# Optimization experiments

Hardware: AMD Instinct MI355X
Metric: run time of the kernel (lower is better)

## Reference

```python
import jax, jax.numpy as jnp
import numpy as np
import math

B, S = 2, 2048
V, D, H, L, DFF = 1024, 512, 8, 6, 2048
DK = D // H
EPS = 1e-5


def _pos_encoding(seq_len, d_model, dtype):
    pos = jnp.arange(seq_len, dtype=jnp.float32)[:, None]
    div = jnp.exp(jnp.arange(0, d_model, 2, dtype=jnp.float32) * (-math.log(10000.0) / d_model))
    pe = jnp.zeros((seq_len, d_model), dtype=jnp.float32)
    pe = pe.at[:, 0::2].set(jnp.sin(pos * div))
    pe = pe.at[:, 1::2].set(jnp.cos(pos * div))
    return pe.astype(dtype)


def _layernorm(x, w, b):
    mu = jnp.mean(x, axis=-1, keepdims=True)
    var = jnp.mean(jnp.square(x - mu), axis=-1, keepdims=True)
    return (x - mu) * jax.lax.rsqrt(var + EPS) * w + b


def setup_inputs() -> dict:
    key = jax.random.key(0)
    ks = jax.random.split(key, 20)
    s = 0.02
    inp = {
        "input_ids": jax.random.randint(ks[0], (B, S), 1, V),
        "emb": jax.random.normal(ks[1], (V, D)) * s,
        # linear weights stored (in, out) so y = x @ W + b
        "wq": jax.random.normal(ks[2], (L, D, D)) * s,
        "bq": jnp.zeros((L, D)),
        "wk": jax.random.normal(ks[3], (L, D, D)) * s,
        "bk": jnp.zeros((L, D)),
        "wv": jax.random.normal(ks[4], (L, D, D)) * s,
        "bv": jnp.zeros((L, D)),
        "wo": jax.random.normal(ks[5], (L, D, D)) * (s / math.sqrt(2 * L)),
        "bo": jnp.zeros((L, D)),
        "ln1_w": jnp.ones((L, D)), "ln1_b": jnp.zeros((L, D)),
        "ln2_w": jnp.ones((L, D)), "ln2_b": jnp.zeros((L, D)),
        "w1": jax.random.normal(ks[6], (L, D, DFF)) * s,
        "b1": jnp.zeros((L, DFF)),
        "w2": jax.random.normal(ks[7], (L, DFF, D)) * (s / math.sqrt(2 * L)),
        "b2": jnp.zeros((L, D)),
        "out_w": jax.random.normal(ks[8], (D, V)) * s,
        "out_b": jnp.zeros((V,)),
    }
    return inp


def reference(input_ids, emb, wq, bq, wk, bk, wv, bv, wo, bo,
              ln1_w, ln1_b, ln2_w, ln2_b, w1, b1, w2, b2, out_w, out_b):
    pad_mask = (input_ids != 0)                              # [B,S] attend where True
    x = emb[input_ids]                                       # [B,S,D]
    x = x + _pos_encoding(S, D, x.dtype)[None, :, :]
    causal = jnp.tril(jnp.ones((S, S), dtype=bool))          # [S,S]
    mask = causal[None, None, :, :] & pad_mask[:, None, None, :]  # [B,1,S,S]
    scale = 1.0 / math.sqrt(DK)
    for l in range(L):
        h = _layernorm(x, ln1_w[l], ln1_b[l])
        q = (h @ wq[l] + bq[l]).reshape(B, S, H, DK)
        k = (h @ wk[l] + bk[l]).reshape(B, S, H, DK)
        v = (h @ wv[l] + bv[l]).reshape(B, S, H, DK)
        scores = jnp.einsum('bqhd,bkhd->bhqk', q, k) * scale
        scores = jnp.where(mask, scores, -jnp.inf)
        attn = jax.nn.softmax(scores, axis=-1)
        o = jnp.einsum('bhqk,bkhd->bqhd', attn, v).reshape(B, S, D)
        x = o @ wo[l] + bo[l]                                # NOTE: no residual on attention (faithful)
        h2 = _layernorm(x, ln2_w[l], ln2_b[l])
        ff = jax.nn.relu(h2 @ w1[l] + b1[l]) @ w2[l] + b2[l]
        x = x + ff
    logits = x @ out_w + out_b                               # [B,S,V]
    return logits
```

## Files before the change

kernel.cpp:

```cpp
#include <hip/hip_runtime.h>
#include <hip/hip_bf16.h>

#define B_ 2
#define S_ 2048
#define V_ 1024
#define D_ 512
#define H_ 8
#define L_ 6
#define DFF_ 2048
#define DK_ 64
#define MROWS (B_*S_)
#define NEGINF (-__builtin_inff())

typedef __hip_bfloat16 bf16;
typedef __bf16 bf16x8 __attribute__((ext_vector_type(8)));
typedef float f32x4 __attribute__((ext_vector_type(4)));
typedef unsigned short us8 __attribute__((ext_vector_type(8)));
typedef unsigned short us2 __attribute__((ext_vector_type(2)));

__device__ __forceinline__ float bf2f(unsigned short u) {
    return __uint_as_float(((unsigned int)u) << 16);
}
__device__ __forceinline__ unsigned short f2b(float x) {
    unsigned int u = __float_as_uint(x);
    return (unsigned short)((u + 0x7FFFu + ((u >> 16) & 1u)) >> 16);
}
__device__ __forceinline__ float ldin(const void* p, size_t i, int bf) {
    return bf ? bf2f(((const unsigned short*)p)[i]) : ((const float*)p)[i];
}

__global__ void detect_kernel(const unsigned int* __restrict__ w, int* __restrict__ flag) {
    if (threadIdx.x == 0) flag[0] = (w[0] == 0x3F800000u) ? 0 : 1;
}

__global__ __launch_bounds__(256) void embed_kernel(const int* __restrict__ ids,
        const void* __restrict__ emb, float* __restrict__ x, const int* __restrict__ dtf)
{
    const int bf = dtf[0];
    int tid = blockIdx.x * 256 + threadIdx.x;
    int d = tid % D_;
    int bs = tid / D_;
    int s = bs % S_;
    int id = ids[bs];
    float e = ldin(emb, (size_t)id * D_ + d, bf);
    int i2 = d & ~1;
    float div = expf((float)i2 * (-9.210340371976184f / (float)D_));
    float ang = (float)s * div;
    float pe = (d & 1) ? cosf(ang) : sinf(ang);
    x[tid] = e + pe;
}

__global__ __launch_bounds__(256) void ln_kernel(const float* __restrict__ x,
        const void* __restrict__ w, const void* __restrict__ b, size_t off,
        unsigned short* __restrict__ out, const int* __restrict__ dtf)
{
    const int bf = dtf[0];
    __shared__ float red[256];
    const int row = blockIdx.x;
    const int tid = threadIdx.x;
    const float* xr = x + (size_t)row * D_;
    float v0 = xr[tid], v1 = xr[tid + 256];
    red[tid] = v0 + v1; __syncthreads();
    for (int s = 128; s > 0; s >>= 1) { if (tid < s) red[tid] += red[tid + s]; __syncthreads(); }
    float mu = red[0] * (1.f / D_); __syncthreads();
    float d0 = v0 - mu, d1 = v1 - mu;
    red[tid] = d0 * d0 + d1 * d1; __syncthreads();
    for (int s = 128; s > 0; s >>= 1) { if (tid < s) red[tid] += red[tid + s]; __syncthreads(); }
    float var = red[0] * (1.f / D_);
    float rstd = rsqrtf(var + 1e-5f);
    unsigned short* orow = out + (size_t)row * D_;
    orow[tid]       = f2b(d0 * rstd * ldin(w, off + tid, bf)       + ldin(b, off + tid, bf));
    orow[tid + 256] = f2b(d1 * rstd * ldin(w, off + tid + 256, bf) + ldin(b, off + tid + 256, bf));
}

__device__ __forceinline__ void tr_tile(const void* src, size_t off, int K, int N,
        unsigned short* dst, int k0, int n0, int bf, unsigned short (*T)[72])
{
    const int t = threadIdx.x;
    const int r = t >> 2, c = (t & 3) * 16;
    size_t e = off + (size_t)(k0 + r) * N + n0 + c;
    us8 u0, u1;
    if (bf) {
        u0 = *(const us8*)((const unsigned short*)src + e);
        u1 = *(const us8*)((const unsigned short*)src + e + 8);
    } else {
        const float* p = (const float*)src + e;
        float4 f0 = *(const float4*)p, f1 = *(const float4*)(p + 4);
        float4 f2 = *(const float4*)(p + 8), f3 = *(const float4*)(p + 12);
        u0[0]=f2b(f0.x); u0[1]=f2b(f0.y); u0[2]=f2b(f0.z); u0[3]=f2b(f0.w);
        u0[4]=f2b(f1.x); u0[5]=f2b(f1.y); u0[6]=f2b(f1.z); u0[7]=f2b(f1.w);
        u1[0]=f2b(f2.x); u1[1]=f2b(f2.y); u1[2]=f2b(f2.z); u1[3]=f2b(f2.w);
        u1[4]=f2b(f3.x); u1[5]=f2b(f3.y); u1[6]=f2b(f3.z); u1[7]=f2b(f3.w);
    }
    *(us8*)&T[r][c] = u0;
    *(us8*)&T[r][c + 8] = u1;
    __syncthreads();
    us8 o0, o1;
    #pragma unroll
    for (int i = 0; i < 8; ++i) { o0[i] = T[c + i][r]; o1[i] = T[c + 8 + i][r]; }
    *(us8*)&dst[(size_t)(n0 + r) * K + k0 + c] = o0;
    *(us8*)&dst[(size_t)(n0 + r) * K + k0 + c + 8] = o1;
}

__global__ __launch_bounds__(256) void transpose_all(
        const void* wq, const void* wk, const void* wv, const void* wo,
        const void* w1, const void* w2,
        unsigned short* twq, unsigned short* twk, unsigned short* twv, unsigned short* two,
        unsigned short* tw1, unsigned short* tw2,
        int lbase, int slotmul, const int* __restrict__ dtf)
{
    __shared__ __align__(16) unsigned short T[64][72];
    const int bf = dtf[0];
    const int lrel = blockIdx.x / 768;
    const int within = blockIdx.x % 768;
    const int layer = lbase + lrel;
    const int slot = lrel * slotmul;
    const size_t offQ = (size_t)layer * D_ * D_;
    const size_t offF = (size_t)layer * D_ * DFF_;
    const size_t sQ = (size_t)slot * D_ * D_;
    const size_t sF = (size_t)slot * D_ * DFF_;
    if (within < 256) {
        int sel = within >> 6, tile = within & 63;
        const void* s = sel == 0 ? wq : sel == 1 ? wk : sel == 2 ? wv : wo;
        unsigned short* d = (sel == 0 ? twq : sel == 1 ? twk : sel == 2 ? twv : two) + sQ;
        tr_tile(s, offQ, D_, D_, d, (tile & 7) * 64, (tile >> 3) * 64, bf, T);
    } else if (within < 512) {
        int tile = within - 256;
        tr_tile(w1, offF, D_, DFF_, tw1 + sF, (tile & 7) * 64, (tile >> 3) * 64, bf, T);
    } else {
        int tile = within - 512;
        tr_tile(w2, offF, DFF_, D_, tw2 + sF, (tile & 31) * 64, (tile >> 5) * 64, bf, T);
    }
}

__global__ __launch_bounds__(256) void transpose_one(const void* src, size_t off,
        int K, int N, unsigned short* dst, const int* __restrict__ dtf)
{
    __shared__ __align__(16) unsigned short T[64][72];
    int tile = blockIdx.x;
    int tk = K / 64;
    tr_tile(src, off, K, N, dst, (tile % tk) * 64, (tile / tk) * 64, dtf[0], T);
}

template<bool ABF16, int OUTM, bool RELU, bool ADD>
__device__ __forceinline__ void gemm_core64(
        const void* __restrict__ A, const unsigned short* __restrict__ Wt,
        const void* __restrict__ bias, size_t bOff, const float* __restrict__ Res,
        void* __restrict__ Cout, int M, int N, int K, int bf)
{
    __shared__ __align__(16) unsigned short At[64][72];
    __shared__ __align__(16) unsigned short Bt[64][72];
    const int tid = threadIdx.x;
    const int wave = tid >> 6, lane = tid & 63;
    const int quad = lane >> 4, l16 = lane & 15;
    const int wm = (wave >> 1) * 32, wn = (wave & 1) * 32;
    const int n0 = blockIdx.x * 64, m0 = blockIdx.y * 64;
    const int r = tid >> 2, cb = tid & 3;

    f32x4 acc[2][2];
    #pragma unroll
    for (int mt = 0; mt < 2; ++mt)
        #pragma unroll
        for (int nt = 0; nt < 2; ++nt)
            acc[mt][nt] = (f32x4){0.f, 0.f, 0.f, 0.f};

    us8 aR[2], wR[2];
    float4 aF[4];

    auto loadT = [&](int k0) {
        if (ABF16) {
            const unsigned short* Ap = (const unsigned short*)A + (size_t)(m0 + r) * K + k0;
            aR[0] = *(const us8*)(Ap + cb * 8);
            aR[1] = *(const us8*)(Ap + (cb + 4) * 8);
        } else {
            const float* Ap = (const float*)A + (size_t)(m0 + r) * K + k0;
            aF[0] = *(const float4*)(Ap + cb * 8);
            aF[1] = *(const float4*)(Ap + cb * 8 + 4);
            aF[2] = *(const float4*)(Ap + (cb + 4) * 8);
            aF[3] = *(const float4*)(Ap + (cb + 4) * 8 + 4);
        }
        const unsigned short* Wp = Wt + (size_t)(n0 + r) * K + k0;
        wR[0] = *(const us8*)(Wp + cb * 8);
        wR[1] = *(const us8*)(Wp + (cb + 4) * 8);
    };
    auto storeT = [&]() {
        if (ABF16) {
            *(us8*)&At[r][cb * 8] = aR[0];
            *(us8*)&At[r][(cb + 4) * 8] = aR[1];
        } else {
            us8 u0, u1;
            u0[0]=f2b(aF[0].x); u0[1]=f2b(aF[0].y); u0[2]=f2b(aF[0].z); u0[3]=f2b(aF[0].w);
            u0[4]=f2b(aF[1].x); u0[5]=f2b(aF[1].y); u0[6]=f2b(aF[1].z); u0[7]=f2b(aF[1].w);
            u1[0]=f2b(aF[2].x); u1[1]=f2b(aF[2].y); u1[2]=f2b(aF[2].z); u1[3]=f2b(aF[2].w);
            u1[4]=f2b(aF[3].x); u1[5]=f2b(aF[3].y); u1[6]=f2b(aF[3].z); u1[7]=f2b(aF[3].w);
            *(us8*)&At[r][cb * 8] = u0;
            *(us8*)&At[r][(cb + 4) * 8] = u1;
        }
        *(us8*)&Bt[r][cb * 8] = wR[0];
        *(us8*)&Bt[r][(cb + 4) * 8] = wR[1];
    };

    loadT(0);
    for (int k0 = 0; k0 < K; k0 += 64) {
        __syncthreads();
        storeT();
        __syncthreads();
        if (k0 + 64 < K) loadT(k0 + 64);
        bf16x8 af[2][2], bw[2][2];
        #pragma unroll
        for (int mt = 0; mt < 2; ++mt)
            #pragma unroll
            for (int kh = 0; kh < 2; ++kh)
                af[mt][kh] = *(const bf16x8*)&At[wm + mt * 16 + l16][kh * 32 + quad * 8];
        #pragma unroll
        for (int nt = 0; nt < 2; ++nt)
            #pragma unroll
            for (int kh = 0; kh < 2; ++kh)
                bw[nt][kh] = *(const bf16x8*)&Bt[wn + nt * 16 + l16][kh * 32 + quad * 8];
        #pragma unroll
        for (int mt = 0; mt < 2; ++mt)
            #pragma unroll
            for (int nt = 0; nt < 2; ++nt) {
                acc[mt][nt] = __builtin_amdgcn_mfma_f32_16x16x32_bf16(af[mt][0], bw[nt][0], acc[mt][nt], 0, 0, 0);
                acc[mt][nt] = __builtin_amdgcn_mfma_f32_16x16x32_bf16(af[mt][1], bw[nt][1], acc[mt][nt], 0, 0, 0);
            }
    }

    #pragma unroll
    for (int mt = 0; mt < 2; ++mt) {
        #pragma unroll
        for (int nt = 0; nt < 2; ++nt) {
            int col = n0 + wn + nt * 16 + l16;
            float bv = ldin(bias, bOff + col, bf);
            #pragma unroll
            for (int rr = 0; rr < 4; ++rr) {
                int row = m0 + wm + mt * 16 + quad * 4 + rr;
                float c = acc[mt][nt][rr] + bv;
                if (ADD) c += Res[(size_t)row * N + col];
                if (RELU) c = fmaxf(c, 0.f);
                if (OUTM == 0)      ((float*)Cout)[(size_t)row * N + col] = c;
                else if (OUTM == 1) ((unsigned short*)Cout)[(size_t)row * N + col] = f2b(c);
                else {
                    if (bf) ((unsigned short*)Cout)[(size_t)row * N + col] = f2b(c);
                    else    ((float*)Cout)[(size_t)row * N + col] = c;
                }
            }
        }
    }
}

template<bool ABF16, int OUTM, bool RELU, bool ADD>
__global__ __launch_bounds__(256) void gemm64(
        const void* __restrict__ A, const unsigned short* __restrict__ Wt,
        const void* __restrict__ bias, size_t bOff, const float* __restrict__ Res,
        void* __restrict__ Cout, int M, int N, int K, const int* __restrict__ dtf)
{
    gemm_core64<ABF16, OUTM, RELU, ADD>(A, Wt, bias, bOff, Res, Cout, M, N, K, dtf[0]);
}

__global__ __launch_bounds__(256) void gemm_qkv64(
        const unsigned short* __restrict__ h,
        const unsigned short* twq, const unsigned short* twk, const unsigned short* twv,
        const void* bq, const void* bk, const void* bv, size_t bOff,
        unsigned short* q, unsigned short* k, unsigned short* v,
        const int* __restrict__ dtf)
{
    const int z = blockIdx.z;
    const unsigned short* W = (z == 0) ? twq : (z == 1) ? twk : twv;
    const void* bias = (z == 0) ? bq : (z == 1) ? bk : bv;
    unsigned short* out = (z == 0) ? q : (z == 1) ? k : v;
    gemm_core64<true, 1, false, false>(h, W, bias, bOff, nullptr, out, MROWS, D_, D_, dtf[0]);
}

__global__ __launch_bounds__(256) void attn_flash_v3(
        const unsigned short* __restrict__ qb, const unsigned short* __restrict__ kb,
        const unsigned short* __restrict__ vb, const int* __restrict__ ids,
        unsigned short* __restrict__ ob)
{
    __shared__ __align__(16) unsigned short Qs[64][72];
    __shared__ __align__(16) unsigned short Ks[2][64][72];
    __shared__ __align__(16) unsigned short Vt[2][64][72];
    __shared__ __align__(16) unsigned short Ps[64][72];
    __shared__ float Msk[S_];
    const int tid = threadIdx.x;
    const int wave = tid >> 6, lane = tid & 63;
    const int quad = lane >> 4, l16 = lane & 15;
    const int pidx = blockIdx.x, h = blockIdx.y, b = blockIdx.z;
    const size_t hb = (size_t)b * S_ * D_ + (size_t)h * DK_;
    const int sr = tid >> 2, scq = (tid & 3) * 16;
    const int pr = tid >> 3, cvb = tid & 7;

    for (int i = tid; i < S_; i += 256)
        Msk[i] = (ids[b * S_ + i] == 0) ? NEGINF : 0.f;

    us8 kR0, kR1, vA, vB;
    auto loadKV = [&](int kt) {
        const unsigned short* kp = kb + hb + (size_t)(kt * 64 + sr) * D_ + scq;
        kR0 = *(const us8*)kp;
        kR1 = *(const us8*)(kp + 8);
        const unsigned short* vp = vb + hb + (size_t)(kt * 64 + 2 * pr) * D_ + cvb * 8;
        vA = *(const us8*)vp;
        vB = *(const us8*)(vp + D_);
    };
    auto storeKV = [&](int buf) {
        *(us8*)&Ks[buf][sr][scq]     = kR0;
        *(us8*)&Ks[buf][sr][scq + 8] = kR1;
        #pragma unroll
        for (int i = 0; i < 8; ++i) {
            int ii = (i + cvb) & 7;
            us2 u2 = { vA[ii], vB[ii] };
            *(us2*)&Vt[buf][cvb * 8 + ii][2 * pr] = u2;
        }
    };

    const int qts[2] = { pidx, 31 - pidx };
    #pragma unroll 1
    for (int pass = 0; pass < 2; ++pass) {
        const int qt = qts[pass];
        __syncthreads();
        {
            const unsigned short* qp = qb + hb + (size_t)(qt * 64 + sr) * D_ + scq;
            *(us8*)&Qs[sr][scq]     = *(const us8*)qp;
            *(us8*)&Qs[sr][scq + 8] = *(const us8*)(qp + 8);
        }
        f32x4 Oa[4];
        float m[4], l[4];
        #pragma unroll
        for (int r = 0; r < 4; ++r) { m[r] = NEGINF; l[r] = 0.f; }
        #pragma unroll
        for (int dt = 0; dt < 4; ++dt) Oa[dt] = (f32x4){0.f, 0.f, 0.f, 0.f};

        loadKV(0);
        storeKV(0);
        if (qt >= 1) loadKV(1);
        __syncthreads();

        #pragma unroll 1
        for (int kt = 0; kt <= qt; ++kt) {
            const int cur = kt & 1;
            f32x4 sa[4];
            #pragma unroll
            for (int nt = 0; nt < 4; ++nt) sa[nt] = (f32x4){0.f, 0.f, 0.f, 0.f};
            #pragma unroll
            for (int ks = 0; ks < 2; ++ks) {
                bf16x8 aq = *(const bf16x8*)&Qs[wave * 16 + l16][ks * 32 + quad * 8];
                #pragma unroll
                for (int nt = 0; nt < 4; ++nt) {
                    bf16x8 bk = *(const bf16x8*)&Ks[cur][nt * 16 + l16][ks * 32 + quad * 8];
                    sa[nt] = __builtin_amdgcn_mfma_f32_16x16x32_bf16(aq, bk, sa[nt], 0, 0, 0);
                }
            }
            #pragma unroll
            for (int r = 0; r < 4; ++r) {
                float sv[4];
                #pragma unroll
                for (int nt = 0; nt < 4; ++nt) {
                    float s = sa[nt][r] * 0.125f + Msk[kt * 64 + nt * 16 + l16];
                    if (kt == qt && (nt * 16 + l16) > (wave * 16 + quad * 4 + r)) s = NEGINF;
                    sv[nt] = s;
                }
                float rmax = fmaxf(fmaxf(sv[0], sv[1]), fmaxf(sv[2], sv[3]));
                #pragma unroll
                for (int off = 8; off > 0; off >>= 1)
                    rmax = fmaxf(rmax, __shfl_xor(rmax, off, 16));
                float mnew = fmaxf(m[r], rmax);
                float alpha = __expf(m[r] - mnew);
                float p[4];
                float rsum = 0.f;
                #pragma unroll
                for (int nt = 0; nt < 4; ++nt) { p[nt] = __expf(sv[nt] - mnew); rsum += p[nt]; }
                #pragma unroll
                for (int off = 8; off > 0; off >>= 1)
                    rsum += __shfl_xor(rsum, off, 16);
                l[r] = l[r] * alpha + rsum;
                m[r] = mnew;
                #pragma unroll
                for (int dt = 0; dt < 4; ++dt) Oa[dt][r] *= alpha;
                int prow = wave * 16 + quad * 4 + r;
                #pragma unroll
                for (int nt = 0; nt < 4; ++nt)
                    Ps[prow][nt * 16 + l16] = f2b(p[nt]);
            }
            #pragma unroll
            for (int ks = 0; ks < 2; ++ks) {
                bf16x8 ap = *(const bf16x8*)&Ps[wave * 16 + l16][ks * 32 + quad * 8];
                #pragma unroll
                for (int dt = 0; dt < 4; ++dt) {
                    bf16x8 bv = *(const bf16x8*)&Vt[cur][dt * 16 + l16][ks * 32 + quad * 8];
                    Oa[dt] = __builtin_amdgcn_mfma_f32_16x16x32_bf16(ap, bv, Oa[dt], 0, 0, 0);
                }
            }
            if (kt + 1 <= qt) {
                storeKV(cur ^ 1);
                if (kt + 2 <= qt) loadKV(kt + 2);
                __syncthreads();
            }
        }
        #pragma unroll
        for (int r = 0; r < 4; ++r) {
            float inv = 1.f / l[r];
            int row = qt * 64 + wave * 16 + quad * 4 + r;
            #pragma unroll
            for (int dt = 0; dt < 4; ++dt)
                ob[hb + (size_t)row * D_ + dt * 16 + l16] = f2b(Oa[dt][r] * inv);
        }
    }
}

extern "C" void kernel_launch(void* const* d_in, const int* in_sizes, int n_in,
                              void* d_out, int out_size, void* d_ws, size_t ws_size,
                              hipStream_t stream)
{
    const int* ids  = (const int*)d_in[0];
    const void* emb = d_in[1];
    const void* wq  = d_in[2];
    const void* bq  = d_in[3];
    const void* wk  = d_in[4];
    const void* bk  = d_in[5];
    const void* wv  = d_in[6];
    const void* bv  = d_in[7];
    const void* wo  = d_in[8];
    const void* bo  = d_in[9];
    const void* ln1w = d_in[10];
    const void* ln1b = d_in[11];
    const void* ln2w = d_in[12];
    const void* ln2b = d_in[13];
    const void* w1  = d_in[14];
    const void* b1  = d_in[15];
    const void* w2  = d_in[16];
    const void* b2  = d_in[17];
    const void* outw = d_in[18];
    const void* outb = d_in[19];

    char* wsp = (char*)d_ws;
    int* dtf = (int*)wsp;
    const size_t NROW = (size_t)MROWS * D_;

    const size_t fixedBytes = 256
        + 2 * NROW * 4
        + 5 * NROW * 2
        + (size_t)MROWS * DFF_ * 2
        + (size_t)D_ * V_ * 2;
    const size_t perLayerW = (4 * (size_t)D_ * D_ + 2 * (size_t)D_ * DFF_) * 2;
    const int slots = (ws_size >= fixedBytes + 6 * perLayerW) ? 6 : 1;

    float* xA = (float*)(wsp + 256);
    float* xB = xA + NROW;
    unsigned short* h  = (unsigned short*)(xB + NROW);
    unsigned short* q  = h + NROW;
    unsigned short* k  = q + NROW;
    unsigned short* v  = k + NROW;
    unsigned short* o  = v + NROW;
    unsigned short* ff = o + NROW;
    unsigned short* twout = ff + (size_t)MROWS * DFF_;
    unsigned short* twq = twout + (size_t)D_ * V_;
    unsigned short* twk = twq + (size_t)slots * D_ * D_;
    unsigned short* twv = twk + (size_t)slots * D_ * D_;
    unsigned short* two = twv + (size_t)slots * D_ * D_;
    unsigned short* tw1 = two + (size_t)slots * D_ * D_;
    unsigned short* tw2 = tw1 + (size_t)slots * D_ * DFF_;

    detect_kernel<<<1, 64, 0, stream>>>((const unsigned int*)ln1w, dtf);
    transpose_one<<<(D_/64) * (V_/64), 256, 0, stream>>>(outw, 0, D_, V_, twout, dtf);
    if (slots == 6)
        transpose_all<<<6 * 768, 256, 0, stream>>>(wq, wk, wv, wo, w1, w2,
            twq, twk, twv, two, tw1, tw2, 0, 1, dtf);
    embed_kernel<<<(MROWS * D_) / 256, 256, 0, stream>>>(ids, emb, xA, dtf);

    for (int l = 0; l < L_; ++l) {
        const size_t bOff = (size_t)l * D_;
        const int s = (slots == 6) ? l : 0;
        if (slots == 1)
            transpose_all<<<768, 256, 0, stream>>>(wq, wk, wv, wo, w1, w2,
                twq, twk, twv, two, tw1, tw2, l, 0, dtf);
        const unsigned short* lwq = twq + (size_t)s * D_ * D_;
        const unsigned short* lwk = twk + (size_t)s * D_ * D_;
        const unsigned short* lwv = twv + (size_t)s * D_ * D_;
        const unsigned short* lwo = two + (size_t)s * D_ * D_;
        const unsigned short* lw1 = tw1 + (size_t)s * D_ * DFF_;
        const unsigned short* lw2 = tw2 + (size_t)s * D_ * DFF_;

        ln_kernel<<<MROWS, 256, 0, stream>>>(xA, ln1w, ln1b, bOff, h, dtf);
        gemm_qkv64<<<dim3(D_/64, MROWS/64, 3), 256, 0, stream>>>(
            h, lwq, lwk, lwv, bq, bk, bv, bOff, q, k, v, dtf);
        attn_flash_v3<<<dim3(S_/128, H_, B_), 256, 0, stream>>>(q, k, v, ids, o);
        gemm64<true, 0, false, false><<<dim3(D_/64, MROWS/64), 256, 0, stream>>>(
            o, lwo, bo, bOff, nullptr, xB, MROWS, D_, D_, dtf);
        ln_kernel<<<MROWS, 256, 0, stream>>>(xB, ln2w, ln2b, bOff, h, dtf);
        gemm64<true, 1, true, false><<<dim3(DFF_/64, MROWS/64), 256, 0, stream>>>(
            h, lw1, b1, (size_t)l * DFF_, nullptr, ff, MROWS, DFF_, D_, dtf);
        gemm64<true, 0, false, true><<<dim3(D_/64, MROWS/64), 256, 0, stream>>>(
            ff, lw2, b2, bOff, xB, xA, MROWS, D_, DFF_, dtf);
    }
    gemm64<false, 2, false, false><<<dim3(V_/64, MROWS/64), 256, 0, stream>>>(
        xA, twout, outb, 0, nullptr, d_out, MROWS, V_, D_, dtf);
}
```

Baseline: 1.054 ms.

## Process both paired query tiles concurrently in a 512-thread attention block

The attention kernel now runs two 256-thread groups per block, one per query tile of the (p, 31-p) pair, instead of processing the two tiles one after the other. In the first phase both groups share the K/V tiles they both need, with the loading split between the groups. In the second phase the long tile's remaining KV range is split across both groups, and the partial softmax states are merged through shared memory with a log-sum-exp combine. This aims to double the waves per block and cut the serial latency of each block. In exchange it adds more shared memory, extra barriers and a merge step, which may lower occupancy.

```diff
diff --git a/kernel.cpp b/kernel.cpp
--- a/kernel.cpp
+++ b/kernel.cpp
@@ -272,29 +272,64 @@
     gemm_core64<true, 1, false, false>(h, W, bias, bOff, nullptr, out, MROWS, D_, D_, dtf[0]);
 }
 
-__global__ __launch_bounds__(256) void attn_flash_v3(
+__global__ __launch_bounds__(512) void attn_flash_v5(
         const unsigned short* __restrict__ qb, const unsigned short* __restrict__ kb,
         const unsigned short* __restrict__ vb, const int* __restrict__ ids,
         unsigned short* __restrict__ ob)
 {
-    __shared__ __align__(16) unsigned short Qs[64][72];
-    __shared__ __align__(16) unsigned short Ks[2][64][72];
-    __shared__ __align__(16) unsigned short Vt[2][64][72];
-    __shared__ __align__(16) unsigned short Ps[64][72];
+    __shared__ __align__(16) unsigned short Qs[2][64][72];
+    __shared__ __align__(16) unsigned short Ks[4][64][72];
+    __shared__ __align__(16) unsigned short Vt[4][64][72];
+    __shared__ __align__(16) unsigned short Ps[2][64][72];
     __shared__ float Msk[S_];
     const int tid = threadIdx.x;
-    const int wave = tid >> 6, lane = tid & 63;
+    const int grp = tid >> 8;
+    const int t = tid & 255;
+    const int wave = t >> 6, lane = t & 63;
     const int quad = lane >> 4, l16 = lane & 15;
-    const int pidx = blockIdx.x, h = blockIdx.y, b = blockIdx.z;
-    const size_t hb = (size_t)b * S_ * D_ + (size_t)h * DK_;
-    const int sr = tid >> 2, scq = (tid & 3) * 16;
-    const int pr = tid >> 3, cvb = tid & 7;
-
-    for (int i = tid; i < S_; i += 256)
-        Msk[i] = (ids[b * S_ + i] == 0) ? NEGINF : 0.f;
+    const int p = blockIdx.x, h = blockIdx.y, bz = blockIdx.z;
+    const int a = p, bqt = 31 - p;
+    const int qt_mine = grp ? bqt : a;
+    const size_t hb = (size_t)bz * S_ * D_ + (size_t)h * DK_;
+    const int sr = t >> 2, scq = (t & 3) * 16;
+    const int pr = t >> 3, cvb = t & 7;
+
+    const int kcols = (bqt + 1) * 64;
+    for (int i = tid; i < kcols; i += 512)
+        Msk[i] = (ids[bz * S_ + i] == 0) ? NEGINF : 0.f;
+
+    {
+        const unsigned short* qp = qb + hb + (size_t)(qt_mine * 64 + sr) * D_ + scq;
+        *(us8*)&Qs[grp][sr][scq]     = *(const us8*)qp;
+        *(us8*)&Qs[grp][sr][scq + 8] = *(const us8*)(qp + 8);
+    }
 
     us8 kR0, kR1, vA, vB;
-    auto loadKV = [&](int kt) {
+    auto loadKV1 = [&](int kt) {
+        if (grp == 0) {
+            const unsigned short* kp = kb + hb + (size_t)(kt * 64 + sr) * D_ + scq;
+            kR0 = *(const us8*)kp;
+            kR1 = *(const us8*)(kp + 8);
+        } else {
+            const unsigned short* vp = vb + hb + (size_t)(kt * 64 + 2 * pr) * D_ + cvb * 8;
+            vA = *(const us8*)vp;
+            vB = *(const us8*)(vp + D_);
+        }
+    };
+    auto storeKV1 = [&](int buf) {
+        if (grp == 0) {
+            *(us8*)&Ks[buf][sr][scq]     = kR0;
+            *(us8*)&Ks[buf][sr][scq + 8] = kR1;
+        } else {
+            #pragma unroll
+            for (int i = 0; i < 8; ++i) {
+                int ii = (i + cvb) & 7;
+                us2 u2 = { vA[ii], vB[ii] };
+                *(us2*)&Vt[buf][cvb * 8 + ii][2 * pr] = u2;
+            }
+        }
+    };
+    auto loadKV2 = [&](int kt) {
         const unsigned short* kp = kb + hb + (size_t)(kt * 64 + sr) * D_ + scq;
         kR0 = *(const us8*)kp;
         kR1 = *(const us8*)(kp + 8);
@@ -302,7 +337,7 @@
         vA = *(const us8*)vp;
         vB = *(const us8*)(vp + D_);
     };
-    auto storeKV = [&](int buf) {
+    auto storeKV2 = [&](int buf) {
         *(us8*)&Ks[buf][sr][scq]     = kR0;
         *(us8*)&Ks[buf][sr][scq + 8] = kR1;
         #pragma unroll
@@ -313,89 +348,68 @@
         }
     };
 
-    const int qts[2] = { pidx, 31 - pidx };
-    #pragma unroll 1
-    for (int pass = 0; pass < 2; ++pass) {
-        const int qt = qts[pass];
-        __syncthreads();
-        {
-            const unsigned short* qp = qb + hb + (size_t)(qt * 64 + sr) * D_ + scq;
-            *(us8*)&Qs[sr][scq]     = *(const us8*)qp;
-            *(us8*)&Qs[sr][scq + 8] = *(const us8*)(qp + 8);
-        }
-        f32x4 Oa[4];
-        float m[4], l[4];
-        #pragma unroll
-        for (int r = 0; r < 4; ++r) { m[r] = NEGINF; l[r] = 0.f; }
-        #pragma unroll
-        for (int dt = 0; dt < 4; ++dt) Oa[dt] = (f32x4){0.f, 0.f, 0.f, 0.f};
-
-        loadKV(0);
-        storeKV(0);
-        if (qt >= 1) loadKV(1);
-        __syncthreads();
-
-        #pragma unroll 1
-        for (int kt = 0; kt <= qt; ++kt) {
-            const int cur = kt & 1;
-            f32x4 sa[4];
-            #pragma unroll
-            for (int nt = 0; nt < 4; ++nt) sa[nt] = (f32x4){0.f, 0.f, 0.f, 0.f};
-            #pragma unroll
-            for (int ks = 0; ks < 2; ++ks) {
-                bf16x8 aq = *(const bf16x8*)&Qs[wave * 16 + l16][ks * 32 + quad * 8];
-                #pragma unroll
-                for (int nt = 0; nt < 4; ++nt) {
-                    bf16x8 bk = *(const bf16x8*)&Ks[cur][nt * 16 + l16][ks * 32 + quad * 8];
-                    sa[nt] = __builtin_amdgcn_mfma_f32_16x16x32_bf16(aq, bk, sa[nt], 0, 0, 0);
-                }
+    f32x4 Oa[4];
+    float m[4], l[4];
+    #pragma unroll
+    for (int r = 0; r < 4; ++r) { m[r] = NEGINF; l[r] = 0.f; }
+    #pragma unroll
+    for (int dt = 0; dt < 4; ++dt) Oa[dt] = (f32x4){0.f, 0.f, 0.f, 0.f};
+
+    auto stepCompute = [&](int qsel, int kt, int buf, bool causal) {
+        f32x4 sa[4];
+        #pragma unroll
+        for (int nt = 0; nt < 4; ++nt) sa[nt] = (f32x4){0.f, 0.f, 0.f, 0.f};
+        #pragma unroll
+        for (int ks = 0; ks < 2; ++ks) {
+            bf16x8 aq = *(const bf16x8*)&Qs[qsel][wave * 16 + l16][ks * 32 + quad * 8];
+            #pragma unroll
+            for (int nt = 0; nt < 4; ++nt) {
+                bf16x8 bk = *(const bf16x8*)&Ks[buf][nt * 16 + l16][ks * 32 + quad * 8];
+                sa[nt] = __builtin_amdgcn_mfma_f32_16x16x32_bf16(aq, bk, sa[nt], 0, 0, 0);
             }
-            #pragma unroll
-            for (int r = 0; r < 4; ++r) {
-                float sv[4];
-                #pragma unroll
-                for (int nt = 0; nt < 4; ++nt) {
-                    float s = sa[nt][r] * 0.125f + Msk[kt * 64 + nt * 16 + l16];
-                    if (kt == qt && (nt * 16 + l16) > (wave * 16 + quad * 4 + r)) s = NEGINF;
-                    sv[nt] = s;
-                }
-                float rmax = fmaxf(fmaxf(sv[0], sv[1]), fmaxf(sv[2], sv[3]));
-                #pragma unroll
-                for (int off = 8; off > 0; off >>= 1)
-                    rmax = fmaxf(rmax, __shfl_xor(rmax, off, 16));
-                float mnew = fmaxf(m[r], rmax);
-                float alpha = __expf(m[r] - mnew);
-                float p[4];
-                float rsum = 0.f;
-                #pragma unroll
-                for (int nt = 0; nt < 4; ++nt) { p[nt] = __expf(sv[nt] - mnew); rsum += p[nt]; }
-                #pragma unroll
-                for (int off = 8; off > 0; off >>= 1)
-                    rsum += __shfl_xor(rsum, off, 16);
-                l[r] = l[r] * alpha + rsum;
-                m[r] = mnew;
-                #pragma unroll
-                for (int dt = 0; dt < 4; ++dt) Oa[dt][r] *= alpha;
-                int prow = wave * 16 + quad * 4 + r;
-                #pragma unroll
-                for (int nt = 0; nt < 4; ++nt)
-                    Ps[prow][nt * 16 + l16] = f2b(p[nt]);
+        }
+        #pragma unroll
+        for (int r = 0; r < 4; ++r) {
+            float sv[4];
+            #pragma unroll
+            for (int nt = 0; nt < 4; ++nt) {
+                float s = sa[nt][r] * 0.125f + Msk[kt * 64 + nt * 16 + l16];
+                if (causal && (nt * 16 + l16) > (wave * 16 + quad * 4 + r)) s = NEGINF;
+                sv[nt] = s;
             }
-            #pragma unroll
-            for (int ks = 0; ks < 2; ++ks) {
-                bf16x8 ap = *(const bf16x8*)&Ps[wave * 16 + l16][ks * 32 + quad * 8];
-                #pragma unroll
-                for (int dt = 0; dt < 4; ++dt) {
-                    bf16x8 bv = *(const bf16x8*)&Vt[cur][dt * 16 + l16][ks * 32 + quad * 8];
-                    Oa[dt] = __builtin_amdgcn_mfma_f32_16x16x32_bf16(ap, bv, Oa[dt], 0, 0, 0);
-                }
+            float rmax = fmaxf(fmaxf(sv[0], sv[1]), fmaxf(sv[2], sv[3]));
+            #pragma unroll
+            for (int off = 8; off > 0; off >>= 1)
+                rmax = fmaxf(rmax, __shfl_xor(rmax, off, 16));
+            float mnew = fmaxf(m[r], rmax);
+            float alpha = __expf(m[r] - mnew);
+            float pv[4];
+            float rsum = 0.f;
+            #pragma unroll
+            for (int nt = 0; nt < 4; ++nt) { pv[nt] = __expf(sv[nt] - mnew); rsum += pv[nt]; }
+            #pragma unroll
+            for (int off = 8; off > 0; off >>= 1)
+                rsum += __shfl_xor(rsum, off, 16);
+            l[r] = l[r] * alpha + rsum;
+            m[r] = mnew;
+            #pragma unroll
+            for (int dt = 0; dt < 4; ++dt) Oa[dt][r] *= alpha;
+            int prow = wave * 16 + quad * 4 + r;
+            #pragma unroll
+            for (int nt = 0; nt < 4; ++nt)
+                Ps[grp][prow][nt * 16 + l16] = f2b(pv[nt]);
+        }
+        #pragma unroll
+        for (int ks = 0; ks < 2; ++ks) {
+            bf16x8 ap = *(const bf16x8*)&Ps[grp][wave * 16 + l16][ks * 32 + quad * 8];
+            #pragma unroll
+            for (int dt = 0; dt < 4; ++dt) {
+                bf16x8 bv = *(const bf16x8*)&Vt[buf][dt * 16 + l16][ks * 32 + quad * 8];
+                Oa[dt] = __builtin_amdgcn_mfma_f32_16x16x32_bf16(ap, bv, Oa[dt], 0, 0, 0);
             }
-            if (kt + 1 <= qt) {
-                storeKV(cur ^ 1);
-                if (kt + 2 <= qt) loadKV(kt + 2);
-                __syncthreads();
-            }
-        }
+        }
+    };
+    auto writeOut = [&](int qt) {
         #pragma unroll
         for (int r = 0; r < 4; ++r) {
             float inv = 1.f / l[r];
@@ -404,6 +418,74 @@
             for (int dt = 0; dt < 4; ++dt)
                 ob[hb + (size_t)row * D_ + dt * 16 + l16] = f2b(Oa[dt][r] * inv);
         }
+    };
+
+    loadKV1(0);
+    storeKV1(0);
+    if (a >= 1) loadKV1(1);
+    __syncthreads();
+
+    #pragma unroll 1
+    for (int kt = 0; kt <= a; ++kt) {
+        const int cur = kt & 1;
+        stepCompute(grp, kt, cur, kt == qt_mine);
+        if (kt + 1 <= a) {
+            storeKV1(cur ^ 1);
+            if (kt + 2 <= a) loadKV1(kt + 2);
+            __syncthreads();
+        }
+    }
+    __syncthreads();
+
+    if (grp == 0) {
+        writeOut(a);
+        #pragma unroll
+        for (int r = 0; r < 4; ++r) { m[r] = NEGINF; l[r] = 0.f; }
+        #pragma unroll
+        for (int dt = 0; dt < 4; ++dt) Oa[dt] = (f32x4){0.f, 0.f, 0.f, 0.f};
+    }
+
+    const int nA = 15 - p, nSteps = 16 - p;
+    auto activeP2 = [&](int step) { return grp ? (step < nSteps) : (step < nA); };
+    auto ktP2 = [&](int step) { return grp ? (16 + step) : (p + 1 + step); };
+
+    if (activeP2(0)) { loadKV2(ktP2(0)); storeKV2(2 * grp); }
+    if (activeP2(1)) loadKV2(ktP2(1));
+    __syncthreads();
+
+    #pragma unroll 1
+    for (int step = 0; step < nSteps; ++step) {
+        if (activeP2(step))
+            stepCompute(1, ktP2(step), 2 * grp + (step & 1), ktP2(step) == bqt);
+        if (step + 1 < nSteps) {
+            if (activeP2(step + 1)) storeKV2(2 * grp + ((step + 1) & 1));
+            if (step + 2 < nSteps && activeP2(step + 2)) loadKV2(ktP2(step + 2));
+        }
+        __syncthreads();
+    }
+
+    float* Ob_ = (float*)&Qs[0][0][0];
+    float* Ml_ = (float*)&Ps[0][0][0];
+    if (grp == 0) {
+        #pragma unroll
+        for (int r = 0; r < 4; ++r) { Ml_[t * 4 + r] = m[r]; Ml_[1024 + t * 4 + r] = l[r]; }
+        #pragma unroll
+        for (int dt = 0; dt < 4; ++dt) *(f32x4*)&Ob_[(dt * 256 + t) * 4] = Oa[dt];
+    }
+    __syncthreads();
+    if (grp == 1) {
+        #pragma unroll
+        for (int r = 0; r < 4; ++r) {
+            float mA = Ml_[t * 4 + r], lA = Ml_[1024 + t * 4 + r];
+            float mN = fmaxf(m[r], mA);
+            float eB = __expf(m[r] - mN), eA = __expf(mA - mN);
+            l[r] = l[r] * eB + lA * eA;
+            m[r] = mN;
+            #pragma unroll
+            for (int dt = 0; dt < 4; ++dt)
+                Oa[dt][r] = Oa[dt][r] * eB + Ob_[(dt * 256 + t) * 4 + r] * eA;
+        }
+        writeOut(bqt);
     }
 }
 
@@ -483,7 +565,7 @@
         ln_kernel<<<MROWS, 256, 0, stream>>>(xA, ln1w, ln1b, bOff, h, dtf);
         gemm_qkv64<<<dim3(D_/64, MROWS/64, 3), 256, 0, stream>>>(
             h, lwq, lwk, lwv, bq, bk, bv, bOff, q, k, v, dtf);
-        attn_flash_v3<<<dim3(S_/128, H_, B_), 256, 0, stream>>>(q, k, v, ids, o);
+        attn_flash_v5<<<dim3(S_/128, H_, B_), 512, 0, stream>>>(q, k, v, ids, o);
         gemm64<true, 0, false, false><<<dim3(D_/64, MROWS/64), 256, 0, stream>>>(
             o, lwo, bo, bOff, nullptr, xB, MROWS, D_, D_, dtf);
         ln_kernel<<<MROWS, 256, 0, stream>>>(xB, ln2w, ln2b, bOff, h, dtf);
```

Measured after the change: 1.037 ms. About the same (-1.6%).
